# Kernel optimization log

Measured on AMD Instinct MI355X. Metric: run time of the kernel, lower is better.

Reference implementation:

```python
import jax, jax.numpy as jnp
import numpy as np

B, C, D, H, W = 4, 64, 64, 64, 64
EPS = 1e-5

def setup_inputs() -> dict:
    key = jax.random.key(0)
    ks = jax.random.split(key, 10)
    s = 1.0 / np.sqrt(C)
    so = 1.0 / np.sqrt(D)
    return {
        "x": jax.random.normal(ks[0], (B, C, H, W), jnp.float32),
        "gn_weight": jnp.ones((C,), jnp.float32),
        "gn_bias": jnp.zeros((C,), jnp.float32),
        "wq": jax.random.uniform(ks[1], (D, C), jnp.float32, -s, s),
        "bq": jax.random.uniform(ks[2], (D,), jnp.float32, -s, s),
        "wk": jax.random.uniform(ks[3], (D, C), jnp.float32, -s, s),
        "bk": jax.random.uniform(ks[4], (D,), jnp.float32, -s, s),
        "wv": jax.random.uniform(ks[5], (D, C), jnp.float32, -s, s),
        "bv": jax.random.uniform(ks[6], (D,), jnp.float32, -s, s),
        "wo": jax.random.uniform(ks[7], (D, D), jnp.float32, -so, so),
        "bo": jax.random.uniform(ks[8], (D,), jnp.float32, -so, so),
    }

def reference(x, gn_weight, gn_bias, wq, bq, wk, bk, wv, bv, wo, bo):
    # GroupNorm with num_groups == channels: per (batch, channel) norm over H,W
    mu = jnp.mean(x, axis=(2, 3), keepdims=True)
    var = jnp.var(x, axis=(2, 3), keepdims=True)
    xn = (x - mu) * jax.lax.rsqrt(var + EPS)
    xn = xn * gn_weight[None, :, None, None] + gn_bias[None, :, None, None]

    # 1x1 convs == channel matmuls; flatten spatial: bcn
    xf = xn.reshape(B, C, H * W)
    Q = jnp.einsum('dc,bcn->bdn', wq, xf) + bq[None, :, None]
    K = jnp.einsum('dc,bcn->bdn', wk, xf) + bk[None, :, None]
    V = jnp.einsum('dc,bcn->bdn', wv, xf) + bv[None, :, None]

    scale = 1.0 / jnp.sqrt(jnp.asarray(D, x.dtype))
    aff = jnp.einsum('bdn,bdm->bnm', Q, K) * scale  # [B, N, N]
    aff = jax.nn.softmax(aff, axis=2)
    att = jnp.einsum('bnm,bdm->bdn', aff, V)  # [B, D, N]

    out = jnp.einsum('ed,bdn->ben', wo, att) + bo[None, :, None]
    return out.reshape(B, D, H, W)
```

## Files before the change

kernel.cpp:

```cpp
#include <hip/hip_runtime.h>


#define B_ 4
#define C_ 64
#define D_ 64
#define N_ 4096

using bf16x8 = __attribute__((ext_vector_type(8))) short;
using u16x8  = __attribute__((ext_vector_type(8))) unsigned short;
using u32x4  = __attribute__((ext_vector_type(4))) unsigned int;
using f32x16 = __attribute__((ext_vector_type(16))) float;
using h16x8  = __attribute__((ext_vector_type(8))) _Float16;

__device__ __forceinline__ unsigned short f2bf(float f) {
    unsigned u = __builtin_bit_cast(unsigned, f);
    u = (u + 0x7FFFu + ((u >> 16) & 1u)) >> 16;
    return (unsigned short)u;
}

#if __has_builtin(__builtin_amdgcn_exp2f)
__device__ __forceinline__ float fast_exp2(float x) {
    return __builtin_amdgcn_exp2f(x);
}
#else
__device__ __forceinline__ float fast_exp2(float x) {
    float r;
    asm volatile("v_exp_f32 %0, %1\n\ts_nop 1" : "=v"(r) : "v"(x));
    return r;
}
#endif

__device__ __forceinline__ void gload16(const void* g, void* l) {
    __builtin_amdgcn_global_load_lds(
        (const __attribute__((address_space(1))) unsigned int*)g,
        (__attribute__((address_space(3))) unsigned int*)l, 16, 0, 0);
}

__global__ __launch_bounds__(1024)
void gn_stats_kernel(const float* __restrict__ x, float* __restrict__ stats) {
    __shared__ float red[32];
    const int bx  = blockIdx.x;
    const int tid = threadIdx.x;
    const float4* xp = (const float4*)(x + (size_t)bx * N_);
    float4 v = xp[tid];
    float s = (v.x + v.y) + (v.z + v.w);
    float q = (v.x * v.x + v.y * v.y) + (v.z * v.z + v.w * v.w);
#pragma unroll
    for (int off = 1; off < 64; off <<= 1) {
        s += __shfl_xor(s, off);
        q += __shfl_xor(q, off);
    }
    const int w = tid >> 6;
    if ((tid & 63) == 0) { red[w * 2] = s; red[w * 2 + 1] = q; }
    __syncthreads();
    if (w == 0) {
        const int lane = tid & 63;
        float sl = (lane < 16) ? red[lane * 2] : 0.f;
        float ql = (lane < 16) ? red[lane * 2 + 1] : 0.f;
#pragma unroll
        for (int off = 1; off < 16; off <<= 1) {
            sl += __shfl_xor(sl, off);
            ql += __shfl_xor(ql, off);
        }
        if (lane == 0) {
            float mu  = sl * (1.f / 4096.f);
            float var = ql * (1.f / 4096.f) - mu * mu;
            var = fmaxf(var, 0.f);
            stats[bx * 2]     = mu;
            stats[bx * 2 + 1] = 1.f / sqrtf(var + 1e-5f);
        }
    }
}

__global__ __launch_bounds__(512)
void gn_qkv_kernel(const float* __restrict__ x, const float* __restrict__ stats,
                   const float* __restrict__ gnw, const float* __restrict__ gnb,
                   const float* __restrict__ wq, const float* __restrict__ bq,
                   const float* __restrict__ wk, const float* __restrict__ bk,
                   const float* __restrict__ wv, const float* __restrict__ bv,
                   unsigned short* __restrict__ Qt, unsigned short* __restrict__ Kf,
                   unsigned short* __restrict__ Vf) {
    __shared__ float xn[64 * 64];
    __shared__ __align__(16) char vs[64 * 128];
    const int t  = threadIdx.x;
    const int bx = blockIdx.x;
    const int b  = bx >> 6;
    const int n0 = (bx & 63) * 64;

    {
        const int c  = t >> 3;
        const int nc = (t & 7) * 8;
        const float* xp = x + (size_t)(b * 64 + c) * N_ + n0 + nc;
        float4 xa = *(const float4*)(xp);
        float4 xb = *(const float4*)(xp + 4);
        float mu = stats[(b * 64 + c) * 2];
        float rs = stats[(b * 64 + c) * 2 + 1];
        float gw = gnw[c] * rs;
        float gb = gnb[c] - mu * gw;
        float* xr = xn + c * 64 + nc;
        xr[0] = xa.x * gw + gb; xr[1] = xa.y * gw + gb;
        xr[2] = xa.z * gw + gb; xr[3] = xa.w * gw + gb;
        xr[4] = xb.x * gw + gb; xr[5] = xb.y * gw + gb;
        xr[6] = xb.z * gw + gb; xr[7] = xb.w * gw + gb;
    }
    __syncthreads();

    const int n    = t & 63;
    const int dblk = __builtin_amdgcn_readfirstlane(t >> 6);
    const int d0   = dblk * 8;

    float aq[8], ak[8], av[8];
#pragma unroll
    for (int i = 0; i < 8; ++i) { aq[i] = 0.f; ak[i] = 0.f; av[i] = 0.f; }

#pragma unroll 4
    for (int c = 0; c < 64; ++c) {
        const float xv = xn[c * 64 + n];
#pragma unroll
        for (int i = 0; i < 8; ++i) {
            aq[i] += wq[(d0 + i) * 64 + c] * xv;
            ak[i] += wk[(d0 + i) * 64 + c] * xv;
            av[i] += wv[(d0 + i) * 64 + c] * xv;
        }
    }

    const float QS = 0.18033688011112042f;
    const int m = n0 + n;
    u16x8 qv, kv, vb;
#pragma unroll
    for (int i = 0; i < 8; ++i) {
        qv[i] = f2bf((aq[i] + bq[d0 + i]) * QS);
        kv[i] = f2bf(ak[i] + bk[d0 + i]);
        vb[i] = f2bf(av[i] + bv[d0 + i]);
    }
    *(u16x8*)(Qt + ((size_t)(b * N_ + m)) * 64 + d0) = qv;
    {
        const int kc = dblk >> 1, h = dblk & 1, mt = m >> 5;
        *(u16x8*)(Kf + ((size_t)((b * 128 + mt) * 4 + kc)) * 512
                     + (h * 32 + (m & 31)) * 8) = kv;
    }
    *(u16x8*)(vs + n * 128 + ((dblk * 16) ^ ((n & 7) << 4))) = vb;
    __syncthreads();

    {
        const int mc_l = t >> 7;
        const int dt   = (t >> 6) & 1;
        const int lp   = t & 63;
        const int hp   = lp >> 5;
        const int dcol = (lp & 31) + dt * 32;
        const int cbase = (dcol & ~7) * 2;
        const int clow  = (dcol & 7) * 2;
        u16x8 tmp;
#pragma unroll
        for (int j = 0; j < 8; ++j) {
            const int ml = mc_l * 16 + hp * 8 + j;
            tmp[j] = *(const unsigned short*)(
                vs + ml * 128 + (cbase ^ (j << 4)) + clow);
        }
        *(u16x8*)(Vf + ((size_t)((b * 256 + (n0 >> 4) + mc_l) * 2 + dt)) * 512
                     + lp * 8) = tmp;
    }
}

__global__ __launch_bounds__(256, 2)
void attn_kernel(const unsigned short* __restrict__ Qt,
                 const unsigned short* __restrict__ Kf,
                 const unsigned short* __restrict__ Vf,
                 _Float16* __restrict__ Opart, float* __restrict__ Lpart,
                 int mspan) {
    __shared__ __align__(16) char smem[2 * 16384];
    const int tid  = threadIdx.x;
    const int lane = tid & 63;
    const int wvu  = __builtin_amdgcn_readfirstlane(tid >> 6);
    const int c    = lane & 31;
    const int h    = lane >> 5;
    const int bid  = blockIdx.x;
    const int b    = bid & 3;
    const int t2   = bid >> 2;
    const int qb   = t2 & 15;
    const int s    = t2 >> 4;
    const int qg0  = qb * 256 + wvu * 64;

    const unsigned short* qp = Qt + (size_t)(b * N_ + qg0 + c) * 64 + h * 8;
    bf16x8 qa0[4], qa1[4];
#pragma unroll
    for (int kc = 0; kc < 4; ++kc) {
        qa0[kc] = *(const bf16x8*)(qp + kc * 16);
        qa1[kc] = *(const bf16x8*)(qp + 32 * 64 + kc * 16);
    }

    f32x16 o00, o01, o10, o11;
#pragma unroll
    for (int i = 0; i < 16; ++i) { o00[i] = 0.f; o01[i] = 0.f; o10[i] = 0.f; o11[i] = 0.f; }
    float lsA0 = 0.f, lsA1 = 0.f, lsB0 = 0.f, lsB1 = 0.f;

    const int NT = mspan >> 6;
    const int mstart = s * mspan;
    const int lof = lane * 16;

    const char* kTn = (const char*)Kf + (size_t)b * 524288
                      + (size_t)(mstart >> 5) * 4096;
    const char* vTn = (const char*)Vf + (size_t)b * 524288
                      + (size_t)(mstart >> 4) * 2048;

    gload16(kTn + (wvu    ) * 1024 + lof, smem + (wvu    ) * 1024);
    gload16(kTn + (wvu + 4) * 1024 + lof, smem + (wvu + 4) * 1024);
    gload16(vTn + (wvu    ) * 1024 + lof, smem + 8192 + (wvu    ) * 1024);
    gload16(vTn + (wvu + 4) * 1024 + lof, smem + 8192 + (wvu + 4) * 1024);
    __syncthreads();

    for (int t = 0; t < NT; ++t) {
        char* buf = smem + ((t & 1) ? 16384 : 0);
        if (t + 1 < NT) {
            kTn += 8192;
            vTn += 8192;
            char* dst = smem + ((t & 1) ? 0 : 16384);
            gload16(kTn + (wvu    ) * 1024 + lof, dst + (wvu    ) * 1024);
            gload16(kTn + (wvu + 4) * 1024 + lof, dst + (wvu + 4) * 1024);
            gload16(vTn + (wvu    ) * 1024 + lof, dst + 8192 + (wvu    ) * 1024);
            gload16(vTn + (wvu + 4) * 1024 + lof, dst + 8192 + (wvu + 4) * 1024);
        }

#pragma unroll
        for (int g = 0; g < 2; ++g) {
            const char* kb = buf + g * 4096 + lof;
            bf16x8 kf0 = *(const bf16x8*)(kb);
            bf16x8 kf1 = *(const bf16x8*)(kb + 1024);
            bf16x8 kf2 = *(const bf16x8*)(kb + 2048);
            bf16x8 kf3 = *(const bf16x8*)(kb + 3072);
            f32x16 sa0, sa1;
#pragma unroll
            for (int i = 0; i < 16; ++i) { sa0[i] = 0.f; sa1[i] = 0.f; }
            sa0 = __builtin_amdgcn_mfma_f32_32x32x16_bf16(kf0, qa0[0], sa0, 0, 0, 0);
            sa1 = __builtin_amdgcn_mfma_f32_32x32x16_bf16(kf0, qa1[0], sa1, 0, 0, 0);
            sa0 = __builtin_amdgcn_mfma_f32_32x32x16_bf16(kf1, qa0[1], sa0, 0, 0, 0);
            sa1 = __builtin_amdgcn_mfma_f32_32x32x16_bf16(kf1, qa1[1], sa1, 0, 0, 0);
            sa0 = __builtin_amdgcn_mfma_f32_32x32x16_bf16(kf2, qa0[2], sa0, 0, 0, 0);
            sa1 = __builtin_amdgcn_mfma_f32_32x32x16_bf16(kf2, qa1[2], sa1, 0, 0, 0);
            sa0 = __builtin_amdgcn_mfma_f32_32x32x16_bf16(kf3, qa0[3], sa0, 0, 0, 0);
            sa1 = __builtin_amdgcn_mfma_f32_32x32x16_bf16(kf3, qa1[3], sa1, 0, 0, 0);

#pragma unroll
            for (int i = 0; i < 16; i += 2) {
                float pA0 = fast_exp2(sa0[i]);
                float pA1 = fast_exp2(sa0[i + 1]);
                float pB0 = fast_exp2(sa1[i]);
                float pB1 = fast_exp2(sa1[i + 1]);
                sa0[i] = pA0; sa0[i + 1] = pA1;
                sa1[i] = pB0; sa1[i + 1] = pB1;
                lsA0 += pA0; lsA1 += pA1;
                lsB0 += pB0; lsB1 += pB1;
            }
            unsigned dwa[8], dwb[8];
#pragma unroll
            for (int i = 0; i < 8; ++i) {
                asm("v_cvt_pk_bf16_f32 %0, %1, %2"
                    : "=v"(dwa[i]) : "v"(sa0[2 * i]), "v"(sa0[2 * i + 1]));
                asm("v_cvt_pk_bf16_f32 %0, %1, %2"
                    : "=v"(dwb[i]) : "v"(sa1[2 * i]), "v"(sa1[2 * i + 1]));
            }
            asm("v_permlane32_swap_b32 %0, %1" : "+v"(dwa[0]), "+v"(dwa[2]));
            asm("v_permlane32_swap_b32 %0, %1" : "+v"(dwa[1]), "+v"(dwa[3]));
            asm("v_permlane32_swap_b32 %0, %1" : "+v"(dwa[4]), "+v"(dwa[6]));
            asm("v_permlane32_swap_b32 %0, %1" : "+v"(dwa[5]), "+v"(dwa[7]));
            asm("v_permlane32_swap_b32 %0, %1" : "+v"(dwb[0]), "+v"(dwb[2]));
            asm("v_permlane32_swap_b32 %0, %1" : "+v"(dwb[1]), "+v"(dwb[3]));
            asm("v_permlane32_swap_b32 %0, %1" : "+v"(dwb[4]), "+v"(dwb[6]));
            asm("v_permlane32_swap_b32 %0, %1" : "+v"(dwb[5]), "+v"(dwb[7]));
            bf16x8 pa0 = __builtin_bit_cast(bf16x8, (u32x4){dwa[0], dwa[1], dwa[2], dwa[3]});
            bf16x8 pa1 = __builtin_bit_cast(bf16x8, (u32x4){dwa[4], dwa[5], dwa[6], dwa[7]});
            bf16x8 pb0 = __builtin_bit_cast(bf16x8, (u32x4){dwb[0], dwb[1], dwb[2], dwb[3]});
            bf16x8 pb1 = __builtin_bit_cast(bf16x8, (u32x4){dwb[4], dwb[5], dwb[6], dwb[7]});

            const char* vb = buf + 8192 + g * 4096 + lof;
            bf16x8 vf0 = *(const bf16x8*)(vb);
            bf16x8 vf1 = *(const bf16x8*)(vb + 1024);
            bf16x8 vf2 = *(const bf16x8*)(vb + 2048);
            bf16x8 vf3 = *(const bf16x8*)(vb + 3072);
            o00 = __builtin_amdgcn_mfma_f32_32x32x16_bf16(vf0, pa0, o00, 0, 0, 0);
            o10 = __builtin_amdgcn_mfma_f32_32x32x16_bf16(vf0, pb0, o10, 0, 0, 0);
            o01 = __builtin_amdgcn_mfma_f32_32x32x16_bf16(vf1, pa0, o01, 0, 0, 0);
            o11 = __builtin_amdgcn_mfma_f32_32x32x16_bf16(vf1, pb0, o11, 0, 0, 0);
            o00 = __builtin_amdgcn_mfma_f32_32x32x16_bf16(vf2, pa1, o00, 0, 0, 0);
            o10 = __builtin_amdgcn_mfma_f32_32x32x16_bf16(vf2, pb1, o10, 0, 0, 0);
            o01 = __builtin_amdgcn_mfma_f32_32x32x16_bf16(vf3, pa1, o01, 0, 0, 0);
            o11 = __builtin_amdgcn_mfma_f32_32x32x16_bf16(vf3, pb1, o11, 0, 0, 0);
        }

        __syncthreads();
    }

    float lsA = lsA0 + lsA1;
    float lsB = lsB0 + lsB1;
    float rsA = lsA + __shfl_xor(lsA, 32);
    float rsB = lsB + __shfl_xor(lsB, 32);

    const size_t s4b = (size_t)(s * 4 + b);
    _Float16* ob = Opart + (s4b * 64 << 12);
#pragma unroll
    for (int r = 0; r < 16; ++r) {
        const int row = (r & 3) + 8 * (r >> 2) + 4 * h;
        ob[((size_t)row << 12) + qg0 + c]             = (_Float16)o00[r];
        ob[((size_t)(row + 32) << 12) + qg0 + c]      = (_Float16)o01[r];
        ob[((size_t)row << 12) + qg0 + 32 + c]        = (_Float16)o10[r];
        ob[((size_t)(row + 32) << 12) + qg0 + 32 + c] = (_Float16)o11[r];
    }
    if (h == 0) {
        Lpart[(s4b << 12) + qg0 + c]      = rsA;
        Lpart[(s4b << 12) + qg0 + 32 + c] = rsB;
    }
}

__global__ __launch_bounds__(256)
void out_proj_kernel(const _Float16* __restrict__ Opart, const float* __restrict__ Lpart,
                     const float* __restrict__ wo, const float* __restrict__ bo,
                     float* __restrict__ out, int S) {
    __shared__ float invl[32];
    __shared__ float attm[64 * 33];
    const int t  = threadIdx.x;
    const int bx = blockIdx.x;
    const int b  = bx >> 7;
    const int n0 = (bx & 127) * 32;

    if (t < 32) {
        float sum = 0.f;
        for (int s = 0; s < S; ++s)
            sum += Lpart[(((size_t)(s * 4 + b)) << 12) + n0 + t];
        invl[t] = 1.f / sum;
    }
    __syncthreads();

    {
        const int d  = t >> 2;
        const int nb = (t & 3) * 8;
        float o[8] = {0.f, 0.f, 0.f, 0.f, 0.f, 0.f, 0.f, 0.f};
        for (int s = 0; s < S; ++s) {
            h16x8 v = *(const h16x8*)(
                Opart + (((size_t)((s * 4 + b) * 64 + d)) << 12) + n0 + nb);
#pragma unroll
            for (int j = 0; j < 8; ++j) o[j] += (float)v[j];
        }
#pragma unroll
        for (int j = 0; j < 8; ++j)
            attm[d * 33 + nb + j] = o[j] * invl[nb + j];
    }
    __syncthreads();

    const int nn = t & 31;
    const int e0 = (t >> 5) * 8;
    float acc[8];
#pragma unroll
    for (int i = 0; i < 8; ++i) acc[i] = bo[e0 + i];
#pragma unroll 8
    for (int d = 0; d < 64; ++d) {
        const float xv = attm[d * 33 + nn];
#pragma unroll
        for (int i = 0; i < 8; ++i) acc[i] += wo[(e0 + i) * 64 + d] * xv;
    }
#pragma unroll
    for (int i = 0; i < 8; ++i)
        out[((size_t)(b * 64 + e0 + i) << 12) + n0 + nn] = acc[i];
}

extern "C" void kernel_launch(void* const* d_in, const int* in_sizes, int n_in,
                              void* d_out, int out_size, void* d_ws, size_t ws_size,
                              hipStream_t stream) {
    const float* x   = (const float*)d_in[0];
    const float* gnw = (const float*)d_in[1];
    const float* gnb = (const float*)d_in[2];
    const float* wq  = (const float*)d_in[3];
    const float* bq  = (const float*)d_in[4];
    const float* wk  = (const float*)d_in[5];
    const float* bk  = (const float*)d_in[6];
    const float* wv  = (const float*)d_in[7];
    const float* bv  = (const float*)d_in[8];
    const float* wo  = (const float*)d_in[9];
    const float* bo  = (const float*)d_in[10];
    float* out = (float*)d_out;

    char* wsb = (char*)d_ws;
    float*          stats = (float*)wsb;
    unsigned short* Qt    = (unsigned short*)(wsb + 2048);
    unsigned short* Kf    = (unsigned short*)(wsb + 2048 + 2097152);
    unsigned short* Vf    = (unsigned short*)(wsb + 2048 + 2 * 2097152);

    const size_t base = 2048 + 3ull * 2097152;
    auto need = [&](int S) {
        return base + (size_t)S * (65536 + 2097152);
    };
    const int S = (ws_size >= need(8)) ? 8
                : (ws_size >= need(4)) ? 4
                : (ws_size >= need(2)) ? 2 : 1;
    const int mspan = N_ / S;
    float*    Lpart = (float*)(wsb + base);
    _Float16* Opart = (_Float16*)(wsb + base + (size_t)S * 65536);

    gn_stats_kernel<<<dim3(B_ * C_), dim3(1024), 0, stream>>>(x, stats);
    gn_qkv_kernel<<<dim3(B_ * 64), dim3(512), 0, stream>>>(
        x, stats, gnw, gnb, wq, bq, wk, bk, wv, bv, Qt, Kf, Vf);
    attn_kernel<<<dim3(16 * 4 * S), dim3(256), 0, stream>>>(
        Qt, Kf, Vf, Opart, Lpart, mspan);
    out_proj_kernel<<<dim3(B_ * 128), dim3(256), 0, stream>>>(
        Opart, Lpart, wo, bo, out, S);
}
```

Baseline: 63.58 us.

## Fuse split-KV merge and output projection into attention kernel with intra-block KV split

Each block now handles 64 queries and splits the KV range across its four waves, each wave double-buffering its own LDS region, so per-wave waitcnt replaces block-level barriers in the main loop. Partial outputs and row sums are merged through LDS and the output projection is applied in the same kernel. This removes the Opart/Lpart global round-trip and the separate out_proj launch. The grid shrinks to 256 blocks using 128KB LDS at occupancy 1, which risks lower latency hiding.

Measured after the change: 61.11 us. -3.9%, faster.

```diff
diff --git a/kernel.cpp b/kernel.cpp
--- a/kernel.cpp
+++ b/kernel.cpp
@@ -10,7 +10,6 @@
 using u16x8  = __attribute__((ext_vector_type(8))) unsigned short;
 using u32x4  = __attribute__((ext_vector_type(4))) unsigned int;
 using f32x16 = __attribute__((ext_vector_type(16))) float;
-using h16x8  = __attribute__((ext_vector_type(8))) _Float16;
 
 __device__ __forceinline__ unsigned short f2bf(float f) {
     unsigned u = __builtin_bit_cast(unsigned, f);
@@ -162,13 +161,13 @@
     }
 }
 
-__global__ __launch_bounds__(256, 2)
+__global__ __launch_bounds__(256, 1)
 void attn_kernel(const unsigned short* __restrict__ Qt,
                  const unsigned short* __restrict__ Kf,
                  const unsigned short* __restrict__ Vf,
-                 _Float16* __restrict__ Opart, float* __restrict__ Lpart,
-                 int mspan) {
-    __shared__ __align__(16) char smem[2 * 16384];
+                 const float* __restrict__ wo, const float* __restrict__ bo,
+                 float* __restrict__ out) {
+    __shared__ __align__(16) char smem[131072];
     const int tid  = threadIdx.x;
     const int lane = tid & 63;
     const int wvu  = __builtin_amdgcn_readfirstlane(tid >> 6);
@@ -176,12 +175,10 @@
     const int h    = lane >> 5;
     const int bid  = blockIdx.x;
     const int b    = bid & 3;
-    const int t2   = bid >> 2;
-    const int qb   = t2 & 15;
-    const int s    = t2 >> 4;
-    const int qg0  = qb * 256 + wvu * 64;
-
-    const unsigned short* qp = Qt + (size_t)(b * N_ + qg0 + c) * 64 + h * 8;
+    const int qc   = bid >> 2;
+    const int n0   = qc * 64;
+
+    const unsigned short* qp = Qt + (size_t)(b * N_ + n0 + c) * 64 + h * 8;
     bf16x8 qa0[4], qa1[4];
 #pragma unroll
     for (int kc = 0; kc < 4; ++kc) {
@@ -194,31 +191,30 @@
     for (int i = 0; i < 16; ++i) { o00[i] = 0.f; o01[i] = 0.f; o10[i] = 0.f; o11[i] = 0.f; }
     float lsA0 = 0.f, lsA1 = 0.f, lsB0 = 0.f, lsB1 = 0.f;
 
-    const int NT = mspan >> 6;
-    const int mstart = s * mspan;
     const int lof = lane * 16;
-
-    const char* kTn = (const char*)Kf + (size_t)b * 524288
-                      + (size_t)(mstart >> 5) * 4096;
-    const char* vTn = (const char*)Vf + (size_t)b * 524288
-                      + (size_t)(mstart >> 4) * 2048;
-
-    gload16(kTn + (wvu    ) * 1024 + lof, smem + (wvu    ) * 1024);
-    gload16(kTn + (wvu + 4) * 1024 + lof, smem + (wvu + 4) * 1024);
-    gload16(vTn + (wvu    ) * 1024 + lof, smem + 8192 + (wvu    ) * 1024);
-    gload16(vTn + (wvu + 4) * 1024 + lof, smem + 8192 + (wvu + 4) * 1024);
-    __syncthreads();
-
-    for (int t = 0; t < NT; ++t) {
-        char* buf = smem + ((t & 1) ? 16384 : 0);
-        if (t + 1 < NT) {
+    char* sbase = smem + wvu * 32768;
+    const char* kTn = (const char*)Kf + (size_t)b * 524288 + (size_t)wvu * 131072;
+    const char* vTn = (const char*)Vf + (size_t)b * 524288 + (size_t)wvu * 131072;
+
+#pragma unroll
+    for (int j = 0; j < 8; ++j) {
+        gload16(kTn + j * 1024 + lof, sbase + j * 1024);
+        gload16(vTn + j * 1024 + lof, sbase + 8192 + j * 1024);
+    }
+    asm volatile("s_waitcnt vmcnt(0)" ::: "memory");
+    __builtin_amdgcn_sched_barrier(0);
+
+    for (int t = 0; t < 16; ++t) {
+        char* buf = sbase + ((t & 1) << 14);
+        if (t + 1 < 16) {
             kTn += 8192;
             vTn += 8192;
-            char* dst = smem + ((t & 1) ? 0 : 16384);
-            gload16(kTn + (wvu    ) * 1024 + lof, dst + (wvu    ) * 1024);
-            gload16(kTn + (wvu + 4) * 1024 + lof, dst + (wvu + 4) * 1024);
-            gload16(vTn + (wvu    ) * 1024 + lof, dst + 8192 + (wvu    ) * 1024);
-            gload16(vTn + (wvu + 4) * 1024 + lof, dst + 8192 + (wvu + 4) * 1024);
+            char* dst = sbase + (((t & 1) ^ 1) << 14);
+#pragma unroll
+            for (int j = 0; j < 8; ++j) {
+                gload16(kTn + j * 1024 + lof, dst + j * 1024);
+                gload16(vTn + j * 1024 + lof, dst + 8192 + j * 1024);
+            }
         }
 
 #pragma unroll
@@ -272,11 +268,11 @@
             bf16x8 pb0 = __builtin_bit_cast(bf16x8, (u32x4){dwb[0], dwb[1], dwb[2], dwb[3]});
             bf16x8 pb1 = __builtin_bit_cast(bf16x8, (u32x4){dwb[4], dwb[5], dwb[6], dwb[7]});
 
-            const char* vb = buf + 8192 + g * 4096 + lof;
-            bf16x8 vf0 = *(const bf16x8*)(vb);
-            bf16x8 vf1 = *(const bf16x8*)(vb + 1024);
-            bf16x8 vf2 = *(const bf16x8*)(vb + 2048);
-            bf16x8 vf3 = *(const bf16x8*)(vb + 3072);
+            const char* vbp = buf + 8192 + g * 4096 + lof;
+            bf16x8 vf0 = *(const bf16x8*)(vbp);
+            bf16x8 vf1 = *(const bf16x8*)(vbp + 1024);
+            bf16x8 vf2 = *(const bf16x8*)(vbp + 2048);
+            bf16x8 vf3 = *(const bf16x8*)(vbp + 3072);
             o00 = __builtin_amdgcn_mfma_f32_32x32x16_bf16(vf0, pa0, o00, 0, 0, 0);
             o10 = __builtin_amdgcn_mfma_f32_32x32x16_bf16(vf0, pb0, o10, 0, 0, 0);
             o01 = __builtin_amdgcn_mfma_f32_32x32x16_bf16(vf1, pa0, o01, 0, 0, 0);
@@ -287,7 +283,8 @@
             o11 = __builtin_amdgcn_mfma_f32_32x32x16_bf16(vf3, pb1, o11, 0, 0, 0);
         }
 
-        __syncthreads();
+        asm volatile("s_waitcnt vmcnt(0)" ::: "memory");
+        __builtin_amdgcn_sched_barrier(0);
     }
 
     float lsA = lsA0 + lsA1;
@@ -295,71 +292,55 @@
     float rsA = lsA + __shfl_xor(lsA, 32);
     float rsB = lsB + __shfl_xor(lsB, 32);
 
-    const size_t s4b = (size_t)(s * 4 + b);
-    _Float16* ob = Opart + (s4b * 64 << 12);
+    __syncthreads();
+    float* mrg   = (float*)smem + wvu * 4096;
+    float* lsm   = (float*)(smem + 65536);
+    float* atile = (float*)(smem + 66560);
 #pragma unroll
     for (int r = 0; r < 16; ++r) {
         const int row = (r & 3) + 8 * (r >> 2) + 4 * h;
-        ob[((size_t)row << 12) + qg0 + c]             = (_Float16)o00[r];
-        ob[((size_t)(row + 32) << 12) + qg0 + c]      = (_Float16)o01[r];
-        ob[((size_t)row << 12) + qg0 + 32 + c]        = (_Float16)o10[r];
-        ob[((size_t)(row + 32) << 12) + qg0 + 32 + c] = (_Float16)o11[r];
+        mrg[row * 64 + c]             = o00[r];
+        mrg[(row + 32) * 64 + c]      = o01[r];
+        mrg[row * 64 + 32 + c]        = o10[r];
+        mrg[(row + 32) * 64 + 32 + c] = o11[r];
     }
     if (h == 0) {
-        Lpart[(s4b << 12) + qg0 + c]      = rsA;
-        Lpart[(s4b << 12) + qg0 + 32 + c] = rsB;
-    }
-}
-
-__global__ __launch_bounds__(256)
-void out_proj_kernel(const _Float16* __restrict__ Opart, const float* __restrict__ Lpart,
-                     const float* __restrict__ wo, const float* __restrict__ bo,
-                     float* __restrict__ out, int S) {
-    __shared__ float invl[32];
-    __shared__ float attm[64 * 33];
-    const int t  = threadIdx.x;
-    const int bx = blockIdx.x;
-    const int b  = bx >> 7;
-    const int n0 = (bx & 127) * 32;
-
-    if (t < 32) {
-        float sum = 0.f;
-        for (int s = 0; s < S; ++s)
-            sum += Lpart[(((size_t)(s * 4 + b)) << 12) + n0 + t];
-        invl[t] = 1.f / sum;
-    }
-    __syncthreads();
-
-    {
-        const int d  = t >> 2;
-        const int nb = (t & 3) * 8;
-        float o[8] = {0.f, 0.f, 0.f, 0.f, 0.f, 0.f, 0.f, 0.f};
-        for (int s = 0; s < S; ++s) {
-            h16x8 v = *(const h16x8*)(
-                Opart + (((size_t)((s * 4 + b) * 64 + d)) << 12) + n0 + nb);
-#pragma unroll
-            for (int j = 0; j < 8; ++j) o[j] += (float)v[j];
-        }
-#pragma unroll
-        for (int j = 0; j < 8; ++j)
-            attm[d * 33 + nb + j] = o[j] * invl[nb + j];
-    }
-    __syncthreads();
-
-    const int nn = t & 31;
-    const int e0 = (t >> 5) * 8;
-    float acc[8];
-#pragma unroll
-    for (int i = 0; i < 8; ++i) acc[i] = bo[e0 + i];
+        lsm[wvu * 64 + c]      = rsA;
+        lsm[wvu * 64 + 32 + c] = rsB;
+    }
+    __syncthreads();
+    {
+        const int dh = wvu >> 1, qh = wvu & 1;
+        const int qq = qh * 32 + c;
+        const float lt = lsm[qq] + lsm[64 + qq] + lsm[128 + qq] + lsm[192 + qq];
+        const float inv = 1.f / lt;
+        const float* m0 = (const float*)smem;
+#pragma unroll
+        for (int r = 0; r < 16; ++r) {
+            const int row = dh * 32 + (r & 3) + 8 * (r >> 2) + 4 * h;
+            const int idx = row * 64 + qq;
+            float sum = (m0[idx] + m0[4096 + idx])
+                      + (m0[8192 + idx] + m0[12288 + idx]);
+            atile[row * 65 + qq] = sum * inv;
+        }
+    }
+    __syncthreads();
+    {
+        const int n  = tid & 63;
+        const int e0 = wvu * 16;
+        float acc[16];
+#pragma unroll
+        for (int i = 0; i < 16; ++i) acc[i] = bo[e0 + i];
 #pragma unroll 8
-    for (int d = 0; d < 64; ++d) {
-        const float xv = attm[d * 33 + nn];
-#pragma unroll
-        for (int i = 0; i < 8; ++i) acc[i] += wo[(e0 + i) * 64 + d] * xv;
-    }
-#pragma unroll
-    for (int i = 0; i < 8; ++i)
-        out[((size_t)(b * 64 + e0 + i) << 12) + n0 + nn] = acc[i];
+        for (int d = 0; d < 64; ++d) {
+            const float xv = atile[d * 65 + n];
+#pragma unroll
+            for (int i = 0; i < 16; ++i) acc[i] += wo[(e0 + i) * 64 + d] * xv;
+        }
+#pragma unroll
+        for (int i = 0; i < 16; ++i)
+            out[((size_t)(b * 64 + e0 + i) << 12) + n0 + n] = acc[i];
+    }
 }
 
 extern "C" void kernel_launch(void* const* d_in, const int* in_sizes, int n_in,
@@ -384,22 +365,9 @@
     unsigned short* Kf    = (unsigned short*)(wsb + 2048 + 2097152);
     unsigned short* Vf    = (unsigned short*)(wsb + 2048 + 2 * 2097152);
 
-    const size_t base = 2048 + 3ull * 2097152;
-    auto need = [&](int S) {
-        return base + (size_t)S * (65536 + 2097152);
-    };
-    const int S = (ws_size >= need(8)) ? 8
-                : (ws_size >= need(4)) ? 4
-                : (ws_size >= need(2)) ? 2 : 1;
-    const int mspan = N_ / S;
-    float*    Lpart = (float*)(wsb + base);
-    _Float16* Opart = (_Float16*)(wsb + base + (size_t)S * 65536);
-
     gn_stats_kernel<<<dim3(B_ * C_), dim3(1024), 0, stream>>>(x, stats);
     gn_qkv_kernel<<<dim3(B_ * 64), dim3(512), 0, stream>>>(
         x, stats, gnw, gnb, wq, bq, wk, bk, wv, bv, Qt, Kf, Vf);
-    attn_kernel<<<dim3(16 * 4 * S), dim3(256), 0, stream>>>(
-        Qt, Kf, Vf, Opart, Lpart, mspan);
-    out_proj_kernel<<<dim3(B_ * 128), dim3(256), 0, stream>>>(
-        Opart, Lpart, wo, bo, out, S);
-}
+    attn_kernel<<<dim3(B_ * 64), dim3(256), 0, stream>>>(
+        Qt, Kf, Vf, wo, bo, out);
+}
```
